# Kernel optimization log

Hardware: AMD Instinct MI355X
Metric: run time of the kernel (lower is better)

Reference implementation:

```python
import jax, jax.numpy as jnp
import numpy as np

B = 256
H, W = 8, 16          # input_resolution for channels=256
C = 768               # dim = channels*3
WS = 4                # window_size
SHIFT = 2             # shift_size
NH = 12               # num_heads
HD = C // NH          # head_dim = 64
HID = 1024            # mlp hidden = channels*4
N = WS * WS           # tokens per window = 16
NW = (H // WS) * (W // WS)  # windows per image = 8
LN_EPS = 1e-5


def _rel_pos_index():
    coords = np.stack(np.meshgrid(np.arange(WS), np.arange(WS), indexing='ij'))  # [2,ws,ws]
    cf = coords.reshape(2, -1)                      # [2, N]
    rel = (cf[:, :, None] - cf[:, None, :]).transpose(1, 2, 0)  # [N, N, 2]
    rel[:, :, 0] += WS - 1
    rel[:, :, 1] += WS - 1
    rel[:, :, 0] *= 2 * WS - 1
    return jnp.asarray(rel.sum(-1))                 # [N, N] int


def _attn_mask():
    img = np.zeros((H, W))
    slices = (slice(0, -WS), slice(-WS, -SHIFT), slice(-SHIFT, None))
    cnt = 0
    for hs in slices:
        for ws_ in slices:
            img[hs, ws_] = cnt
            cnt += 1
    mw = img.reshape(H // WS, WS, W // WS, WS).transpose(0, 2, 1, 3).reshape(-1, N)  # [nW, N]
    am = mw[:, None, :] - mw[:, :, None]            # [nW, N, N]
    return jnp.asarray(np.where(am != 0, -100.0, 0.0).astype(np.float32))


REL_IDX = _rel_pos_index()
ATTN_MASK = _attn_mask()


def _ln(x, g, b):
    m = x.mean(-1, keepdims=True)
    v = ((x - m) ** 2).mean(-1, keepdims=True)
    return (x - m) / jnp.sqrt(v + LN_EPS) * g + b


def setup_inputs() -> dict:
    key = jax.random.key(0)
    ks = jax.random.split(key, 8)
    s = 0.02
    return {
        'x': jax.random.normal(ks[0], (B, H * W, C), jnp.float32),
        'ln1_g': jnp.ones((C,), jnp.float32),
        'ln1_b': jnp.zeros((C,), jnp.float32),
        'qkv_w': jax.random.normal(ks[1], (C, 3 * C), jnp.float32) * s,
        'qkv_b': jnp.zeros((3 * C,), jnp.float32),
        'proj_w': jax.random.normal(ks[2], (C, C), jnp.float32) * s,
        'proj_b': jnp.zeros((C,), jnp.float32),
        'rel_table': jax.random.normal(ks[3], ((2 * WS - 1) * (2 * WS - 1), NH), jnp.float32) * s,
        'ln2_g': jnp.ones((C,), jnp.float32),
        'ln2_b': jnp.zeros((C,), jnp.float32),
        'fc1_w': jax.random.normal(ks[4], (C, HID), jnp.float32) * s,
        'fc1_b': jax.random.normal(ks[5], (HID,), jnp.float32) * 1e-6,
        'fc2_w': jax.random.normal(ks[6], (HID, C), jnp.float32) * s,
        'fc2_b': jax.random.normal(ks[7], (C,), jnp.float32) * 1e-6,
    }


def reference(x, ln1_g, ln1_b, qkv_w, qkv_b, proj_w, proj_b, rel_table,
              ln2_g, ln2_b, fc1_w, fc1_b, fc2_w, fc2_b):
    # --- norm1 + cyclic shift + window partition ---
    h = _ln(x, ln1_g, ln1_b).reshape(B, H, W, C)
    h = jnp.roll(h, (-SHIFT, -SHIFT), axis=(1, 2))
    hw = h.reshape(B, H // WS, WS, W // WS, WS, C).transpose(0, 1, 3, 2, 4, 5)
    hw = hw.reshape(B * NW, N, C)                   # (num_windows*B, N, C)
    # --- window attention with relative position bias + shift mask ---
    qkv = (hw @ qkv_w + qkv_b).reshape(B * NW, N, 3, NH, HD).transpose(2, 0, 3, 1, 4)
    q, k, v = qkv[0] * (HD ** -0.5), qkv[1], qkv[2]  # [Bn, NH, N, HD]
    attn = jnp.einsum('bhnd,bhmd->bhnm', q, k)      # [Bn, NH, N, N]
    bias = rel_table[REL_IDX].transpose(2, 0, 1)    # [NH, N, N]
    attn = attn + bias[None]
    attn = attn.reshape(B, NW, NH, N, N) + ATTN_MASK[None, :, None]
    attn = jax.nn.softmax(attn.reshape(B * NW, NH, N, N), axis=-1)
    o = jnp.einsum('bhnm,bhmd->bhnd', attn, v).transpose(0, 2, 1, 3).reshape(B * NW, N, C)
    o = o @ proj_w + proj_b
    # --- window reverse + reverse shift + residual ---
    o = o.reshape(B, H // WS, W // WS, WS, WS, C).transpose(0, 1, 3, 2, 4, 5).reshape(B, H, W, C)
    o = jnp.roll(o, (SHIFT, SHIFT), axis=(1, 2)).reshape(B, H * W, C)
    x = x + o
    # --- MLP block (dropout is identity at inference) ---
    y = _ln(x, ln2_g, ln2_b)
    y = jax.nn.gelu(y @ fc1_w + fc1_b, approximate=False)
    return x + (y @ fc2_w + fc2_b)
```

## Files before the change

kernel.cpp:

```cpp
#include <hip/hip_runtime.h>
#include <stdint.h>
#include <stddef.h>

typedef __attribute__((ext_vector_type(8))) short bf16x8;
typedef __attribute__((ext_vector_type(4))) float f32x4;
typedef __attribute__((ext_vector_type(4))) unsigned int uint4v;

static __device__ __forceinline__ unsigned short f2bf(float f) {
  unsigned int u = __builtin_bit_cast(unsigned int, f);
  unsigned int r = (u + 0x7FFFu + ((u >> 16) & 1u)) >> 16;
  return (unsigned short)r;
}

static __device__ __forceinline__ void gld16(const void* g, void* l) {
  __builtin_amdgcn_global_load_lds(
      (const __attribute__((address_space(1))) void*)g,
      (__attribute__((address_space(3))) void*)l, 16, 0, 0);
}

__global__ void transpose_cast(const float* __restrict__ src,
                               unsigned short* __restrict__ dst, int R, int C) {
  __shared__ float tile[32][33];
  int c0 = blockIdx.x * 32, r0 = blockIdx.y * 32;
  int tx = threadIdx.x, ty = threadIdx.y;
  #pragma unroll
  for (int i = 0; i < 32; i += 8)
    tile[ty + i][tx] = src[(size_t)(r0 + ty + i) * C + c0 + tx];
  __syncthreads();
  #pragma unroll
  for (int i = 0; i < 32; i += 8)
    dst[(size_t)(c0 + ty + i) * R + r0 + tx] = f2bf(tile[tx][ty + i]);
}

static __device__ __forceinline__ float blksum256(float v, float* sb) {
  #pragma unroll
  for (int o = 32; o > 0; o >>= 1) v += __shfl_down(v, o, 64);
  int lane = threadIdx.x & 63, w = threadIdx.x >> 6;
  __syncthreads();
  if (lane == 0) sb[w] = v;
  __syncthreads();
  return sb[0] + sb[1] + sb[2] + sb[3];
}

template <int MODE>
__global__ __launch_bounds__(256) void ln_kernel(const float* __restrict__ x,
                                                 const float* __restrict__ gg,
                                                 const float* __restrict__ bb,
                                                 unsigned short* __restrict__ out) {
  __shared__ float sb[4];
  const int d = blockIdx.x;
  size_t srow;
  if (MODE == 0) {
    int b = d >> 7, wid = (d >> 4) & 7, tok = d & 15;
    int oh = (((wid >> 2) << 2) + (tok >> 2) + 2) & 7;
    int ow = (((wid & 3) << 2) + (tok & 3) + 2) & 15;
    srow = (size_t)(b << 7) + oh * 16 + ow;
  } else {
    srow = d;
  }
  const float* xr = x + srow * 768;
  const int t = threadIdx.x;
  float v0 = xr[t], v1 = xr[t + 256], v2 = xr[t + 512];
  float mean = blksum256(v0 + v1 + v2, sb) * (1.0f / 768.0f);
  float d0 = v0 - mean, d1 = v1 - mean, d2 = v2 - mean;
  float var = blksum256(d0 * d0 + d1 * d1 + d2 * d2, sb) * (1.0f / 768.0f);
  float rstd = rsqrtf(var + 1e-5f);
  size_t o = (size_t)d * 768;
  out[o + t]       = f2bf(d0 * rstd * gg[t] + bb[t]);
  out[o + t + 256] = f2bf(d1 * rstd * gg[t + 256] + bb[t + 256]);
  out[o + t + 512] = f2bf(d2 * rstd * gg[t + 512] + bb[t + 512]);
}

template <int EPI>
__global__ __launch_bounds__(256) void gemm_bt(const unsigned short* __restrict__ A,
                                               const unsigned short* __restrict__ BT,
                                               const float* __restrict__ bias,
                                               float* __restrict__ outF,
                                               unsigned short* __restrict__ outB,
                                               const float* __restrict__ resid,
                                               int M, int N, int K) {
  __shared__ __align__(16) unsigned short As[128 * 32];
  __shared__ __align__(16) unsigned short Bs[128 * 32];
  const int tid = threadIdx.x;
  const int lane = tid & 63, wv = tid >> 6;
  const int m0 = blockIdx.y << 7, n0 = blockIdx.x << 7;
  const int wr = (wv >> 1) << 6, wc = (wv & 1) << 6;
  const int fr = lane & 15, kg = (lane >> 4) << 3;

  f32x4 acc[4][4];
  #pragma unroll
  for (int i = 0; i < 4; ++i)
    #pragma unroll
    for (int j = 0; j < 4; ++j) acc[i][j] = (f32x4){0.f, 0.f, 0.f, 0.f};

  const int l4 = lane >> 2;
  const int lb = (lane & 3) << 3;
  const unsigned short* gA = A + (size_t)(m0 + wv * 32 + l4) * K + lb;
  const unsigned short* gB = BT + (size_t)(n0 + wv * 32 + l4) * K + lb;
  char* lA = (char*)As + wv * 32 * 64;
  char* lB = (char*)Bs + wv * 32 * 64;

  for (int k0 = 0; k0 < K; k0 += 32) {
    gld16(gA + k0, lA);
    gld16(gA + (size_t)16 * K + k0, lA + 1024);
    gld16(gB + k0, lB);
    gld16(gB + (size_t)16 * K + k0, lB + 1024);
    __syncthreads();
    bf16x8 af[4], bfr[4];
    #pragma unroll
    for (int m = 0; m < 4; ++m)
      af[m] = *(const bf16x8*)&As[(wr + m * 16 + fr) * 32 + kg];
    #pragma unroll
    for (int n = 0; n < 4; ++n)
      bfr[n] = *(const bf16x8*)&Bs[(wc + n * 16 + fr) * 32 + kg];
    #pragma unroll
    for (int m = 0; m < 4; ++m)
      #pragma unroll
      for (int n = 0; n < 4; ++n)
        acc[m][n] = __builtin_amdgcn_mfma_f32_16x16x32_bf16(af[m], bfr[n], acc[m][n], 0, 0, 0);
    __syncthreads();
  }

  #pragma unroll
  for (int mi = 0; mi < 4; ++mi) {
    #pragma unroll
    for (int ni = 0; ni < 4; ++ni) {
      const int col = n0 + wc + ni * 16 + fr;
      const float bc = bias[col];
      #pragma unroll
      for (int i = 0; i < 4; ++i) {
        const int row = m0 + wr + mi * 16 + ((lane >> 4) << 2) + i;
        float v = acc[mi][ni][i] + bc;
        if (EPI == 0) {
          outB[(size_t)row * N + col] = f2bf(v);
        } else if (EPI == 1) {
          int b = row >> 7, wid = (row >> 4) & 7, tok = row & 15;
          int oh = (((wid >> 2) << 2) + (tok >> 2) + 2) & 7;
          int ow = (((wid & 3) << 2) + (tok & 3) + 2) & 15;
          size_t di = ((size_t)(b << 7) + oh * 16 + ow) * 768 + col;
          outF[di] = v + resid[di];
        } else if (EPI == 2) {
          float g = 0.5f * v * (1.0f + erff(v * 0.70710678118f));
          outB[(size_t)row * N + col] = f2bf(g);
        } else {
          size_t di = (size_t)row * N + col;
          outF[di] = v + resid[di];
        }
      }
    }
  }
}

__global__ __launch_bounds__(64) void attn_win(const unsigned short* __restrict__ qkv,
                                               const float* __restrict__ rel_table,
                                               unsigned short* __restrict__ o) {
  __shared__ __align__(16) unsigned short q_s[16 * 64];
  __shared__ __align__(16) unsigned short k_s[16 * 64];
  __shared__ __align__(16) unsigned short vt_s[64 * 32];
  __shared__ __align__(16) unsigned short p_s[16 * 32];
  const int bid = blockIdx.x;
  const int win = bid / 12;
  const int head = bid - win * 12;
  const int wid = win & 7;
  const int lane = threadIdx.x;
  const unsigned short* gq =
      qkv + (size_t)win * 16 * 2304 + head * 64 + (size_t)(lane >> 2) * 2304 + ((lane & 3) << 4);
  const int t = lane >> 2, d0 = (lane & 3) << 4;
  *(uint4v*)&q_s[t * 64 + d0]     = *(const uint4v*)(gq);
  *(uint4v*)&q_s[t * 64 + d0 + 8] = *(const uint4v*)(gq + 8);
  *(uint4v*)&k_s[t * 64 + d0]     = *(const uint4v*)(gq + 768);
  *(uint4v*)&k_s[t * 64 + d0 + 8] = *(const uint4v*)(gq + 776);
  unsigned short vv[16];
  *(uint4v*)&vv[0] = *(const uint4v*)(gq + 1536);
  *(uint4v*)&vv[8] = *(const uint4v*)(gq + 1544);
  #pragma unroll
  for (int e = 0; e < 16; ++e) vt_s[(d0 + e) * 32 + t] = vv[e];
  #pragma unroll
  for (int e = 0; e < 16; ++e) vt_s[lane * 32 + 16 + e] = 0;
  if (lane < 16) {
    #pragma unroll
    for (int e = 0; e < 16; ++e) p_s[lane * 32 + 16 + e] = 0;
  }
  __syncthreads();

  const int fr = lane & 15, kg = (lane >> 4) << 3;
  bf16x8 qa0 = *(const bf16x8*)&q_s[fr * 64 + kg];
  bf16x8 qa1 = *(const bf16x8*)&q_s[fr * 64 + 32 + kg];
  bf16x8 ka0 = *(const bf16x8*)&k_s[fr * 64 + kg];
  bf16x8 ka1 = *(const bf16x8*)&k_s[fr * 64 + 32 + kg];
  f32x4 s = (f32x4){0.f, 0.f, 0.f, 0.f};
  s = __builtin_amdgcn_mfma_f32_16x16x32_bf16(qa0, ka0, s, 0, 0, 0);
  s = __builtin_amdgcn_mfma_f32_16x16x32_bf16(qa1, ka1, s, 0, 0, 0);

  const int wh = wid >> 2, wwc = wid & 3;
  const int rj = fr >> 2, cj = fr & 3;
  const int rowm = wh * 4 + rj, colm = wwc * 4 + cj;
  const int rgm = (rowm < 4 ? 0 : (rowm < 6 ? 1 : 2)) * 3 +
                  (colm < 12 ? 0 : (colm < 14 ? 1 : 2));
  float p[4];
  #pragma unroll
  for (int i = 0; i < 4; ++i) {
    int n = ((lane >> 4) << 2) + i;
    int ri = n >> 2, ci = n & 3;
    int rown = wh * 4 + ri, coln = wwc * 4 + ci;
    int rgn = (rown < 4 ? 0 : (rown < 6 ? 1 : 2)) * 3 +
              (coln < 12 ? 0 : (coln < 14 ? 1 : 2));
    float bias = rel_table[(size_t)((ri - rj + 3) * 7 + (ci - cj + 3)) * 12 + head];
    p[i] = s[i] * 0.125f + bias + (rgn != rgm ? -100.0f : 0.0f);
  }
  float mx[4] = {p[0], p[1], p[2], p[3]};
  #pragma unroll
  for (int off = 8; off > 0; off >>= 1)
    #pragma unroll
    for (int i = 0; i < 4; ++i) mx[i] = fmaxf(mx[i], __shfl_xor(mx[i], off, 64));
  float sm[4];
  #pragma unroll
  for (int i = 0; i < 4; ++i) { p[i] = __expf(p[i] - mx[i]); sm[i] = p[i]; }
  #pragma unroll
  for (int off = 8; off > 0; off >>= 1)
    #pragma unroll
    for (int i = 0; i < 4; ++i) sm[i] += __shfl_xor(sm[i], off, 64);
  #pragma unroll
  for (int i = 0; i < 4; ++i)
    p_s[(((lane >> 4) << 2) + i) * 32 + fr] = f2bf(p[i] / sm[i]);
  __syncthreads();

  bf16x8 pa = *(const bf16x8*)&p_s[fr * 32 + kg];
  const f32x4 oz = (f32x4){0.f, 0.f, 0.f, 0.f};
  #pragma unroll
  for (int c = 0; c < 4; ++c) {
    bf16x8 vb = *(const bf16x8*)&vt_s[(c * 16 + fr) * 32 + kg];
    f32x4 oa = __builtin_amdgcn_mfma_f32_16x16x32_bf16(pa, vb, oz, 0, 0, 0);
    #pragma unroll
    for (int i = 0; i < 4; ++i) {
      int n = ((lane >> 4) << 2) + i;
      o[((size_t)win * 16 + n) * 768 + head * 64 + c * 16 + fr] = f2bf(oa[i]);
    }
  }
}

extern "C" void kernel_launch(void* const* d_in, const int* in_sizes, int n_in,
                              void* d_out, int out_size, void* d_ws, size_t ws_size,
                              hipStream_t stream) {
  const float* x      = (const float*)d_in[0];
  const float* ln1_g  = (const float*)d_in[1];
  const float* ln1_b  = (const float*)d_in[2];
  const float* qkv_w  = (const float*)d_in[3];
  const float* qkv_b  = (const float*)d_in[4];
  const float* proj_w = (const float*)d_in[5];
  const float* proj_b = (const float*)d_in[6];
  const float* rel_t  = (const float*)d_in[7];
  const float* ln2_g  = (const float*)d_in[8];
  const float* ln2_b  = (const float*)d_in[9];
  const float* fc1_w  = (const float*)d_in[10];
  const float* fc1_b  = (const float*)d_in[11];
  const float* fc2_w  = (const float*)d_in[12];
  const float* fc2_b  = (const float*)d_in[13];
  float* out = (float*)d_out;

  char* ws = (char*)d_ws;
  unsigned short* wsA = (unsigned short*)(ws);
  unsigned short* qkvb = (unsigned short*)(ws + 50331648);
  float* xr = (float*)(ws + 50331648);
  unsigned short* h1 = (unsigned short*)(ws + 201326592);
  unsigned short* qkv_wT = (unsigned short*)(ws + 268435456);
  unsigned short* proj_wT = (unsigned short*)(ws + 271974400);
  unsigned short* fc1_wT = (unsigned short*)(ws + 273154048);
  unsigned short* fc2_wT = (unsigned short*)(ws + 274726912);

  dim3 tb(32, 8);
  transpose_cast<<<dim3(2304 / 32, 768 / 32), tb, 0, stream>>>(qkv_w, qkv_wT, 768, 2304);
  transpose_cast<<<dim3(768 / 32, 768 / 32), tb, 0, stream>>>(proj_w, proj_wT, 768, 768);
  transpose_cast<<<dim3(1024 / 32, 768 / 32), tb, 0, stream>>>(fc1_w, fc1_wT, 768, 1024);
  transpose_cast<<<dim3(768 / 32, 1024 / 32), tb, 0, stream>>>(fc2_w, fc2_wT, 1024, 768);

  ln_kernel<0><<<32768, 256, 0, stream>>>(x, ln1_g, ln1_b, wsA);
  gemm_bt<0><<<dim3(18, 256), 256, 0, stream>>>(wsA, qkv_wT, qkv_b, nullptr, qkvb,
                                                nullptr, 32768, 2304, 768);
  attn_win<<<24576, 64, 0, stream>>>(qkvb, rel_t, wsA);
  gemm_bt<1><<<dim3(6, 256), 256, 0, stream>>>(wsA, proj_wT, proj_b, xr, nullptr,
                                               x, 32768, 768, 768);
  ln_kernel<1><<<32768, 256, 0, stream>>>(xr, ln2_g, ln2_b, wsA);
  gemm_bt<2><<<dim3(8, 256), 256, 0, stream>>>(wsA, fc1_wT, fc1_b, nullptr, h1,
                                               nullptr, 32768, 1024, 768);
  gemm_bt<3><<<dim3(6, 256), 256, 0, stream>>>(h1, fc2_wT, fc2_b, out, nullptr,
                                               xr, 32768, 768, 1024);
}
```

Measured before the change: 609.5 us.

## Replace GEMM with 256x256-tile double-buffered swizzled-LDS MFMA kernel

```diff
diff --git a/kernel.cpp b/kernel.cpp
--- a/kernel.cpp
+++ b/kernel.cpp
@@ -72,65 +72,130 @@
 }
 
 template <int EPI>
-__global__ __launch_bounds__(256) void gemm_bt(const unsigned short* __restrict__ A,
-                                               const unsigned short* __restrict__ BT,
-                                               const float* __restrict__ bias,
-                                               float* __restrict__ outF,
-                                               unsigned short* __restrict__ outB,
-                                               const float* __restrict__ resid,
-                                               int M, int N, int K) {
-  __shared__ __align__(16) unsigned short As[128 * 32];
-  __shared__ __align__(16) unsigned short Bs[128 * 32];
+__global__ __launch_bounds__(512, 2) void gemm256(
+    const unsigned short* __restrict__ A, const unsigned short* __restrict__ BT,
+    const float* __restrict__ bias, float* __restrict__ outF,
+    unsigned short* __restrict__ outB, const float* __restrict__ resid,
+    int M, int N, int K, int NT) {
+  __shared__ __align__(16) unsigned short sA[2][256 * 64];
+  __shared__ __align__(16) unsigned short sB[2][256 * 64];
+
   const int tid = threadIdx.x;
   const int lane = tid & 63, wv = tid >> 6;
-  const int m0 = blockIdx.y << 7, n0 = blockIdx.x << 7;
-  const int wr = (wv >> 1) << 6, wc = (wv & 1) << 6;
-  const int fr = lane & 15, kg = (lane >> 4) << 3;
-
-  f32x4 acc[4][4];
-  #pragma unroll
-  for (int i = 0; i < 4; ++i)
+  const int wr = wv >> 2, wc = wv & 3;
+  const int fr = lane & 15, q4 = (lane >> 4) << 2;
+
+  const int nwg = gridDim.x;
+  const int orig = blockIdx.x;
+  const int swz = (orig & 7) * (nwg >> 3) + (orig >> 3);
+  const int mt = swz / NT, nt = swz - mt * NT;
+  const int m0 = mt << 8, n0 = nt << 8;
+
+  const size_t K2 = (size_t)K * 2;
+
+  const int srow = tid >> 3;
+  const int sg = tid & 7;
+  const int sgs = ((sg ^ (srow & 7)) << 4);
+  const char* pA = (const char*)A + (size_t)(m0 + srow) * K2 + sgs;
+  const char* pB = (const char*)BT + (size_t)(n0 + srow) * K2 + sgs;
+  char* lwA[2] = {(char*)&sA[0][0] + (wv << 10), (char*)&sA[1][0] + (wv << 10)};
+  char* lwB[2] = {(char*)&sB[0][0] + (wv << 10), (char*)&sB[1][0] + (wv << 10)};
+
+  const int g0 = (((lane >> 4) ^ (fr & 7)) << 4);
+  const int g1 = (((4 + (lane >> 4)) ^ (fr & 7)) << 4);
+  const int arow = (wr << 7) + fr;
+  const int brow = (wc << 6) + fr;
+
+  f32x4 acc[8][4];
+  #pragma unroll
+  for (int i = 0; i < 8; ++i)
     #pragma unroll
     for (int j = 0; j < 4; ++j) acc[i][j] = (f32x4){0.f, 0.f, 0.f, 0.f};
 
-  const int l4 = lane >> 2;
-  const int lb = (lane & 3) << 3;
-  const unsigned short* gA = A + (size_t)(m0 + wv * 32 + l4) * K + lb;
-  const unsigned short* gB = BT + (size_t)(n0 + wv * 32 + l4) * K + lb;
-  char* lA = (char*)As + wv * 32 * 64;
-  char* lB = (char*)Bs + wv * 32 * 64;
-
-  for (int k0 = 0; k0 < K; k0 += 32) {
-    gld16(gA + k0, lA);
-    gld16(gA + (size_t)16 * K + k0, lA + 1024);
-    gld16(gB + k0, lB);
-    gld16(gB + (size_t)16 * K + k0, lB + 1024);
-    __syncthreads();
-    bf16x8 af[4], bfr[4];
-    #pragma unroll
-    for (int m = 0; m < 4; ++m)
-      af[m] = *(const bf16x8*)&As[(wr + m * 16 + fr) * 32 + kg];
-    #pragma unroll
-    for (int n = 0; n < 4; ++n)
-      bfr[n] = *(const bf16x8*)&Bs[(wc + n * 16 + fr) * 32 + kg];
-    #pragma unroll
-    for (int m = 0; m < 4; ++m)
-      #pragma unroll
-      for (int n = 0; n < 4; ++n)
-        acc[m][n] = __builtin_amdgcn_mfma_f32_16x16x32_bf16(af[m], bfr[n], acc[m][n], 0, 0, 0);
-    __syncthreads();
-  }
-
-  #pragma unroll
-  for (int mi = 0; mi < 4; ++mi) {
-    #pragma unroll
-    for (int ni = 0; ni < 4; ++ni) {
-      const int col = n0 + wc + ni * 16 + fr;
+  bf16x8 af[4][2], bb[2][2];
+  const int KT = K >> 6;
+
+#define STAGE(la, lb, t)                                                   \
+  {                                                                        \
+    const size_t koff = (size_t)(t) << 7;                                  \
+    _Pragma("unroll") for (int j = 0; j < 4; ++j) {                        \
+      gld16(pA + (size_t)(j * 64) * K2 + koff, (la) + j * 8192);           \
+      gld16(pB + (size_t)(j * 64) * K2 + koff, (lb) + j * 8192);           \
+    }                                                                      \
+  }
+
+#define LDA(cbuf, mh)                                                      \
+  {                                                                        \
+    const char* bas = (const char*)&sA[cbuf][0];                           \
+    _Pragma("unroll") for (int fm = 0; fm < 4; ++fm) {                     \
+      const int r = arow + (mh) * 64 + fm * 16;                            \
+      af[fm][0] = *(const bf16x8*)(bas + r * 128 + g0);                    \
+      af[fm][1] = *(const bf16x8*)(bas + r * 128 + g1);                    \
+    }                                                                      \
+  }
+
+#define LDB(cbuf, nh)                                                      \
+  {                                                                        \
+    const char* bas = (const char*)&sB[cbuf][0];                           \
+    _Pragma("unroll") for (int fn = 0; fn < 2; ++fn) {                     \
+      const int r = brow + (nh) * 32 + fn * 16;                            \
+      bb[fn][0] = *(const bf16x8*)(bas + r * 128 + g0);                    \
+      bb[fn][1] = *(const bf16x8*)(bas + r * 128 + g1);                    \
+    }                                                                      \
+  }
+
+#define MMA(mh, nh)                                                        \
+  {                                                                        \
+    __builtin_amdgcn_s_barrier();                                          \
+    __builtin_amdgcn_s_setprio(1);                                         \
+    _Pragma("unroll") for (int fm = 0; fm < 4; ++fm) {                     \
+      _Pragma("unroll") for (int fn = 0; fn < 2; ++fn) {                   \
+        acc[(mh)*4 + fm][(nh)*2 + fn] =                                    \
+            __builtin_amdgcn_mfma_f32_16x16x32_bf16(                       \
+                af[fm][0], bb[fn][0], acc[(mh)*4 + fm][(nh)*2 + fn], 0, 0, 0); \
+        acc[(mh)*4 + fm][(nh)*2 + fn] =                                    \
+            __builtin_amdgcn_mfma_f32_16x16x32_bf16(                       \
+                af[fm][1], bb[fn][1], acc[(mh)*4 + fm][(nh)*2 + fn], 0, 0, 0); \
+      }                                                                    \
+    }                                                                      \
+    __builtin_amdgcn_s_setprio(0);                                         \
+    __builtin_amdgcn_s_barrier();                                          \
+  }
+
+  STAGE(lwA[0], lwB[0], 0);
+  STAGE(lwA[1], lwB[1], 1);
+  asm volatile("s_waitcnt vmcnt(8)" ::: "memory");
+  __builtin_amdgcn_s_barrier();
+
+  for (int t = 0; t < KT; ++t) {
+    const int cur = t & 1;
+    LDA(cur, 0) LDB(cur, 0) MMA(0, 0)
+    LDB(cur, 1) MMA(0, 1)
+    LDA(cur, 1) MMA(1, 1)
+    LDB(cur, 0) MMA(1, 0)
+    if (t + 2 < KT) {
+      STAGE(lwA[cur], lwB[cur], t + 2);
+      asm volatile("s_waitcnt vmcnt(8)" ::: "memory");
+    } else {
+      asm volatile("s_waitcnt vmcnt(0)" ::: "memory");
+    }
+    __builtin_amdgcn_s_barrier();
+  }
+#undef STAGE
+#undef LDA
+#undef LDB
+#undef MMA
+
+  #pragma unroll
+  for (int ai = 0; ai < 8; ++ai) {
+    #pragma unroll
+    for (int bj = 0; bj < 4; ++bj) {
+      const int col = n0 + (wc << 6) + bj * 16 + fr;
       const float bc = bias[col];
       #pragma unroll
       for (int i = 0; i < 4; ++i) {
-        const int row = m0 + wr + mi * 16 + ((lane >> 4) << 2) + i;
-        float v = acc[mi][ni][i] + bc;
+        const int row = m0 + (wr << 7) + ai * 16 + q4 + i;
+        float v = acc[ai][bj][i] + bc;
         if (EPI == 0) {
           outB[(size_t)row * N + col] = f2bf(v);
         } else if (EPI == 1) {
@@ -275,14 +340,14 @@
   transpose_cast<<<dim3(768 / 32, 1024 / 32), tb, 0, stream>>>(fc2_w, fc2_wT, 1024, 768);
 
   ln_kernel<0><<<32768, 256, 0, stream>>>(x, ln1_g, ln1_b, wsA);
-  gemm_bt<0><<<dim3(18, 256), 256, 0, stream>>>(wsA, qkv_wT, qkv_b, nullptr, qkvb,
-                                                nullptr, 32768, 2304, 768);
+  gemm256<0><<<dim3(128 * 9), 512, 0, stream>>>(wsA, qkv_wT, qkv_b, nullptr, qkvb,
+                                                nullptr, 32768, 2304, 768, 9);
   attn_win<<<24576, 64, 0, stream>>>(qkvb, rel_t, wsA);
-  gemm_bt<1><<<dim3(6, 256), 256, 0, stream>>>(wsA, proj_wT, proj_b, xr, nullptr,
-                                               x, 32768, 768, 768);
+  gemm256<1><<<dim3(128 * 3), 512, 0, stream>>>(wsA, proj_wT, proj_b, xr, nullptr,
+                                                x, 32768, 768, 768, 3);
   ln_kernel<1><<<32768, 256, 0, stream>>>(xr, ln2_g, ln2_b, wsA);
-  gemm_bt<2><<<dim3(8, 256), 256, 0, stream>>>(wsA, fc1_wT, fc1_b, nullptr, h1,
-                                               nullptr, 32768, 1024, 768);
-  gemm_bt<3><<<dim3(6, 256), 256, 0, stream>>>(h1, fc2_wT, fc2_b, out, nullptr,
-                                               xr, 32768, 768, 1024);
-}
+  gemm256<2><<<dim3(128 * 4), 512, 0, stream>>>(wsA, fc1_wT, fc1_b, nullptr, h1,
+                                                nullptr, 32768, 1024, 768, 4);
+  gemm256<3><<<dim3(128 * 3), 512, 0, stream>>>(h1, fc2_wT, fc2_b, out, nullptr,
+                                                xr, 32768, 768, 1024, 3);
+}
```

Result: no change. 616.8 us (+1.2%).
